# Kernel tuning notes

Hardware: AMD Instinct MI355X
Metric: run time of the kernel (lower is better)

The kernel has to match this reference:

```python
import jax, jax.numpy as jnp
import numpy as np


def _ste_round(x):
    # Round forward, identity backward (matches the custom torch Round.apply)
    return x + jax.lax.stop_gradient(jnp.round(x) - x)


def setup_inputs() -> dict:
    key = jax.random.key(0)
    k1, k2, k3 = jax.random.split(key, 3)
    N, C, H, W = 32, 256, 56, 56
    x = jax.random.normal(k1, (N, C, H, W), dtype=jnp.float32)
    # orthonormal projection basis, as produced by SVD of the covariance
    u, _ = jnp.linalg.qr(jax.random.normal(k2, (C, C), dtype=jnp.float32))
    # per-channel positive clamp values (Laplace-MSE-optimal in the original)
    clampVal = jax.random.uniform(k3, (C,), dtype=jnp.float32) * 3.0 + 0.5
    return {"x": x, "u": u, "clampVal": clampVal, "actBitwidth": 8}


def reference(x, u, clampVal, actBitwidth):
    N, C, H, W = x.shape
    # relu, then flatten to [C, N*H*W] (channels as rows, like transpose(0,1).view)
    im = jax.nn.relu(x).transpose(1, 0, 2, 3).reshape(C, -1)
    mn = jnp.mean(im, axis=1, keepdims=True)             # per-channel mean [C,1]
    im = im - mn
    # project onto PCA basis: imProj = u^T @ im  -> [C, L]
    p = jnp.matmul(u.T, im)
    # per-channel symmetric clamp (vectorized over the original per-channel loop)
    cv = clampVal[:, None]
    p = jnp.clip(p, -cv, cv)
    if actBitwidth < 17:
        dmax = jnp.max(p, axis=1, keepdims=True)         # dynamic per-channel max
        dmin = jnp.min(p, axis=1, keepdims=True)         # dynamic per-channel min
        same = dmax == dmin
        rng = jnp.where(same, jnp.ones_like(dmax), dmax - dmin)
        levels = jnp.asarray(2 ** actBitwidth - 1, dtype=p.dtype)
        scale = levels / rng
        q = _ste_round((p - dmin) * scale) / scale + dmin
        p = jnp.where(same, p, q)                        # act_quant skips if max==min
    # unproject, recenter, restore original per-channel mean
    p = jnp.matmul(u, p)
    p = p - jnp.mean(p, axis=1, keepdims=True) + mn
    return p.reshape(C, N, H, W).transpose(1, 0, 2, 3)
```

## Files before the change

### kernel.cpp

```cpp
#include <hip/hip_runtime.h>
#include <math.h>

typedef unsigned short ushort;
typedef unsigned int uint;
using half8   = __attribute__((ext_vector_type(8))) _Float16;
using short8  = __attribute__((ext_vector_type(8))) short;
using floatx4 = __attribute__((ext_vector_type(4))) float;

#define CCH   256
#define HWSZ  3136
#define NBAT  32
#define MCOLS (NBAT*HWSZ)
#define MB    784
#define NIB   4
#define GEMMGRID (MB*NIB)
#define CPX  (GEMMGRID/8)
#define QBLKS 1568

#define S_MN     0
#define S_OFFS   256
#define S_DMAX   512
#define S_DMIN   768
#define S_QSUM   1024
#define S_ROWADD 1280
#define S_MEAN   1536
#define S_TOTAL  2048

__device__ __forceinline__ ushort f2h(float f){
    _Float16 h = (_Float16)f;
    return __builtin_bit_cast(ushort, h);
}
__device__ __forceinline__ float h2f(ushort u){
    return (float)__builtin_bit_cast(_Float16, u);
}
__device__ __forceinline__ void atomicMaxF(float* addr, float v){
    if (v >= 0.f) atomicMax((int*)addr, __float_as_int(v));
    else          atomicMin((unsigned*)addr, (unsigned)__float_as_int(v));
}
__device__ __forceinline__ void atomicMinF(float* addr, float v){
    if (v >= 0.f) atomicMin((int*)addr, __float_as_int(v));
    else          atomicMax((unsigned*)addr, (unsigned)__float_as_int(v));
}
__device__ __forceinline__ void gld_lds16(const void* g, void* l){
    __builtin_amdgcn_global_load_lds((const __attribute__((address_space(1))) void*)g,
                                     (__attribute__((address_space(3))) void*)l, 16, 0, 0);
}
__device__ __forceinline__ void xcd_unswizzle(int w, int& bx, int& iy){
    int l = (w & 7)*CPX + (w >> 3);
    bx = l >> 2; iy = l & 3;
}

__global__ void k_init(float* __restrict__ stats){
    int t = blockIdx.x * 256 + threadIdx.x;
    if (t < S_TOTAL){
        float v = 0.f;
        if (t >= S_DMAX && t < S_DMIN)      v = -__builtin_inff();
        else if (t >= S_DMIN && t < S_QSUM) v =  __builtin_inff();
        stats[t] = v;
    }
}

__global__ void k_prep(const float* __restrict__ u, ushort* __restrict__ uTh){
    int i = blockIdx.x, c = threadIdx.x;
    uTh[i*CCH + c] = f2h(u[(size_t)c*CCH + i]);
}

__global__ __launch_bounds__(256) void k_trans(const float* __restrict__ x,
                                               ushort* __restrict__ xT,
                                               float* __restrict__ stats){
    __shared__ ushort tile[64*66];
    __shared__ float csum[64];
    const int hwb = blockIdx.x*64, cb = blockIdx.y*64, n = blockIdx.z;
    const int t = threadIdx.x, lane = t & 63;
    const int hw0 = (t & 15)*4;
    float4 v[4];
    #pragma unroll
    for (int pass = 0; pass < 4; ++pass){
        int c = cb + pass*16 + (t >> 4);
        v[pass] = *(const float4*)&x[((size_t)(n*CCH + c))*HWSZ + hwb + hw0];
    }
    #pragma unroll
    for (int pass = 0; pass < 4; ++pass){
        float a0 = fmaxf(v[pass].x, 0.f), a1 = fmaxf(v[pass].y, 0.f);
        float a2 = fmaxf(v[pass].z, 0.f), a3 = fmaxf(v[pass].w, 0.f);
        int cl = pass*16 + (t >> 4);
        uint p0 = (uint)f2h(a0) | ((uint)f2h(a1) << 16);
        uint p1 = (uint)f2h(a2) | ((uint)f2h(a3) << 16);
        *(uint*)&tile[cl*66 + hw0]     = p0;
        *(uint*)&tile[cl*66 + hw0 + 2] = p1;
        float sv = (a0 + a1) + (a2 + a3);
        #pragma unroll
        for (int o = 1; o < 16; o <<= 1) sv += __shfl_xor(sv, o);
        if ((lane & 15) == 0) csum[cl] = sv;
    }
    __syncthreads();
    {
        int hl = t >> 2, cs = (t & 3)*16;
        short8 o0, o1;
        #pragma unroll
        for (int j = 0; j < 8; ++j) o0[j] = (short)tile[(cs + j)*66 + hl];
        #pragma unroll
        for (int j = 0; j < 8; ++j) o1[j] = (short)tile[(cs + 8 + j)*66 + hl];
        size_t m = (size_t)n*HWSZ + hwb + hl;
        ushort* dst = xT + m*CCH + cb + cs;
        *(short8*)dst       = o0;
        *(short8*)(dst + 8) = o1;
    }
    if (t < 64) atomicAdd(&stats[S_MN + cb + t], csum[t]);
}

__global__ __launch_bounds__(256) void k_stats1(const float* __restrict__ u,
                                                float* __restrict__ stats){
    const int i = blockIdx.x, t = threadIdx.x;
    const float invM = 1.f/(float)MCOLS;
    float mnc  = stats[S_MN + t] * invM;
    float term = u[(size_t)t*CCH + i] * mnc;
    #pragma unroll
    for (int o = 1; o < 64; o <<= 1) term += __shfl_xor(term, o);
    __shared__ float red[4];
    if ((t & 63) == 0) red[t >> 6] = term;
    __syncthreads();
    if (t == 0){
        stats[S_OFFS + i] = red[0] + red[1] + red[2] + red[3];
        stats[S_MEAN + i] = stats[S_MN + i] * invM;
    }
}

__global__ __launch_bounds__(256) void k_gemm1(const ushort* __restrict__ xT,
                                               const ushort* __restrict__ uTh,
                                               const float* __restrict__ clampVal,
                                               const float* __restrict__ stats,
                                               ushort* __restrict__ pT,
                                               float* __restrict__ pmin,
                                               float* __restrict__ pmax){
    __shared__ ushort sU[64*256];
    int bx, iy; xcd_unswizzle(blockIdx.x, bx, iy);
    const int m0 = bx*128, i0 = iy*64;
    const int t = threadIdx.x, lane = t & 63, wm = t >> 6;
    const int col = lane & 15, quad = lane >> 4;
    #pragma unroll
    for (int j = 0; j < 8; ++j){
        int cid = j*256 + t;
        int row = cid >> 5, c = cid & 31;
        gld_lds16(uTh + (size_t)(i0+row)*CCH + ((c ^ (row & 7))*8), sU + cid*8);
    }
    floatx4 acc[4][2] = {};
    __syncthreads();
    const ushort* xbase = xT + (size_t)(m0 + wm*32 + col)*CCH + quad*8;
    #pragma unroll
    for (int ks = 0; ks < 8; ++ks){
        half8 b0 = __builtin_bit_cast(half8, *(const short8*)(xbase + ks*32));
        half8 b1 = __builtin_bit_cast(half8, *(const short8*)(xbase + 16*CCH + ks*32));
        #pragma unroll
        for (int fi = 0; fi < 4; ++fi){
            int chunk = (ks*4 + quad) ^ (col & 7);
            half8 a = __builtin_bit_cast(half8, *(const short8*)(sU + (fi*16 + col)*CCH + chunk*8));
            acc[fi][0] = __builtin_amdgcn_mfma_f32_16x16x32_f16(a, b0, acc[fi][0], 0, 0, 0);
            acc[fi][1] = __builtin_amdgcn_mfma_f32_16x16x32_f16(a, b1, acc[fi][1], 0, 0, 0);
        }
    }
    const int R = (iy*MB + bx)*4 + wm;
    #pragma unroll
    for (int fi = 0; fi < 4; ++fi){
        float off[4], cv[4], mnv[4], mxv[4];
        #pragma unroll
        for (int r = 0; r < 4; ++r){
            int ig = i0 + fi*16 + quad*4 + r;
            off[r] = stats[S_OFFS + ig];
            cv[r]  = clampVal[ig];
            mnv[r] =  __builtin_inff();
            mxv[r] = -__builtin_inff();
        }
        #pragma unroll
        for (int fm = 0; fm < 2; ++fm){
            int m = m0 + wm*32 + fm*16 + col;
            ushort pk[4];
            #pragma unroll
            for (int r = 0; r < 4; ++r){
                float v = acc[fi][fm][r] - off[r];
                v = fminf(fmaxf(v, -cv[r]), cv[r]);
                ushort h = f2h(v);
                float vr = h2f(h);
                pk[r] = h;
                mnv[r] = fminf(mnv[r], vr);
                mxv[r] = fmaxf(mxv[r], vr);
            }
            ushort4 q4 = make_ushort4(pk[0], pk[1], pk[2], pk[3]);
            *(ushort4*)(pT + (size_t)m*CCH + i0 + fi*16 + quad*4) = q4;
        }
        #pragma unroll
        for (int r = 0; r < 4; ++r){
            float mn = mnv[r], mx = mxv[r];
            #pragma unroll
            for (int o = 1; o < 16; o <<= 1){
                mn = fminf(mn, __shfl_xor(mn, o));
                mx = fmaxf(mx, __shfl_xor(mx, o));
            }
            if (col == 0){
                int il = fi*16 + quad*4 + r;
                pmin[(size_t)R*64 + il] = mn;
                pmax[(size_t)R*64 + il] = mx;
            }
        }
    }
}

__global__ __launch_bounds__(64) void k_mmred(const float* __restrict__ pmin,
                                              const float* __restrict__ pmax,
                                              float* __restrict__ stats){
    const int iy = blockIdx.x, sl = blockIdx.y, il = threadIdx.x;
    float mn = __builtin_inff(), mx = -__builtin_inff();
    const int base = iy*3136 + sl*98;
    for (int r = 0; r < 98; ++r){
        mn = fminf(mn, pmin[(size_t)(base + r)*64 + il]);
        mx = fmaxf(mx, pmax[(size_t)(base + r)*64 + il]);
    }
    atomicMinF(&stats[S_DMIN + iy*64 + il], mn);
    atomicMaxF(&stats[S_DMAX + iy*64 + il], mx);
}

__global__ __launch_bounds__(256) void k_prep2(const float* __restrict__ u,
                                               const int* __restrict__ abw,
                                               const float* __restrict__ stats,
                                               ushort* __restrict__ uhs){
    const int i = blockIdx.x, k = threadIdx.x;
    const int ab = *abw;
    const float lv = (float)(((ab < 17) ? (1 << ab) : 2) - 1);
    float dmax = stats[S_DMAX + k], dmin = stats[S_DMIN + k];
    float rng = dmax - dmin;
    bool cen = (ab < 17) && (ab <= 11) && (rng > 0.f);
    float step = cen ? rng / lv : 1.f;
    uhs[(size_t)i*CCH + k] = f2h(u[(size_t)i*CCH + k] * step);
}

__global__ __launch_bounds__(256) void k_qsum(ushort* __restrict__ pT,
                                              const int* __restrict__ abw,
                                              const float* __restrict__ stats,
                                              float* __restrict__ qsump){
    const int t = threadIdx.x, b = blockIdx.x;
    const int ic = (t & 31)*8, ml = t >> 5;
    const int ab = *abw;
    const float lv = (float)(((ab < 17) ? (1 << ab) : 2) - 1);
    const bool cen = (ab < 17) && (ab <= 11);
    const float hl = 0.5f * lv;
    float dmn[8], scl[8], stp[8];
    #pragma unroll
    for (int j = 0; j < 8; ++j){
        float dmax = stats[S_DMAX + ic + j], dmin = stats[S_DMIN + ic + j];
        float rng = dmax - dmin;
        bool doq = (ab < 17) && (rng > 0.f);
        scl[j] = doq ? lv / rng : 0.f;
        stp[j] = doq ? rng / lv : 0.f;
        dmn[j] = dmin;
    }
    float s[8] = {0,0,0,0,0,0,0,0};
    #pragma unroll
    for (int r = 0; r < 8; ++r){
        int m = b*64 + r*8 + ml;
        ushort* prow = pT + (size_t)m*CCH + ic;
        short8 pv = *(const short8*)prow;
        short8 ov;
        #pragma unroll
        for (int j = 0; j < 8; ++j){
            float f = h2f((ushort)pv[j]);
            float bv;
            if (scl[j] > 0.f){
                float n = rintf((f - dmn[j])*scl[j]);
                bv = cen ? (n - hl)
                         : h2f(f2h(fmaf(n, stp[j], dmn[j])));
            } else bv = f;
            ov[j] = (short)f2h(bv);
            s[j] += bv;
        }
        *(short8*)prow = ov;
    }
    __shared__ float red[256*8];
    #pragma unroll
    for (int j = 0; j < 8; ++j) red[(ic + j)*8 + ml] = s[j];
    __syncthreads();
    float tot = 0.f;
    #pragma unroll
    for (int q = 0; q < 8; ++q) tot += red[t*8 + q];
    qsump[(size_t)b*256 + t] = tot;
}

__global__ __launch_bounds__(256) void k_stats2a(const float* __restrict__ qsump,
                                                 float* __restrict__ stats){
    const int k = blockIdx.x, t = threadIdx.x;
    float s = 0.f;
    for (int b = t; b < QBLKS; b += 256) s += qsump[(size_t)b*256 + k];
    #pragma unroll
    for (int o = 1; o < 64; o <<= 1) s += __shfl_xor(s, o);
    __shared__ float red[4];
    if ((t & 63) == 0) red[t >> 6] = s;
    __syncthreads();
    if (t == 0) stats[S_QSUM + k] = (red[0]+red[1]+red[2]+red[3]) * (1.f/(float)MCOLS);
}

__global__ __launch_bounds__(256) void k_stats2b(const ushort* __restrict__ uhs,
                                                 float* __restrict__ stats){
    const int i = blockIdx.x, t = threadIdx.x;
    float term = h2f(uhs[(size_t)i*CCH + t]) * stats[S_QSUM + t];
    #pragma unroll
    for (int o = 1; o < 64; o <<= 1) term += __shfl_xor(term, o);
    __shared__ float red[4];
    if ((t & 63) == 0) red[t >> 6] = term;
    __syncthreads();
    if (t == 0) stats[S_ROWADD + i] = stats[S_MEAN + i] - (red[0]+red[1]+red[2]+red[3]);
}

__global__ __launch_bounds__(256) void k_gemm2(const ushort* __restrict__ pT,
                                               const ushort* __restrict__ uhs,
                                               float* __restrict__ out,
                                               const float* __restrict__ stats){
    __shared__ ushort sU[64*256];
    int bx, iy; xcd_unswizzle(blockIdx.x, bx, iy);
    const int m0 = bx*128, i0 = iy*64;
    const int t = threadIdx.x, lane = t & 63, wm = t >> 6;
    const int col = lane & 15, quad = lane >> 4;
    #pragma unroll
    for (int j = 0; j < 8; ++j){
        int cid = j*256 + t;
        int row = cid >> 5, c = cid & 31;
        gld_lds16(uhs + (size_t)(i0+row)*CCH + ((c ^ (row & 7))*8), sU + cid*8);
    }
    floatx4 acc[4][2] = {};
    __syncthreads();
    const ushort* pbase = pT + (size_t)(m0 + wm*32 + col)*CCH + quad*8;
    #pragma unroll
    for (int ks = 0; ks < 8; ++ks){
        half8 b0 = __builtin_bit_cast(half8, *(const short8*)(pbase + ks*32));
        half8 b1 = __builtin_bit_cast(half8, *(const short8*)(pbase + 16*CCH + ks*32));
        #pragma unroll
        for (int fi = 0; fi < 4; ++fi){
            int chunk = (ks*4 + quad) ^ (col & 7);
            half8 a = __builtin_bit_cast(half8, *(const short8*)(sU + (fi*16 + col)*CCH + chunk*8));
            acc[fi][0] = __builtin_amdgcn_mfma_f32_16x16x32_f16(a, b0, acc[fi][0], 0, 0, 0);
            acc[fi][1] = __builtin_amdgcn_mfma_f32_16x16x32_f16(a, b1, acc[fi][1], 0, 0, 0);
        }
    }
    float* sF = (float*)sU;
    const int rl = t >> 4, c4 = (t & 15)*4;
    #pragma unroll
    for (int p = 0; p < 2; ++p){
        __syncthreads();
        #pragma unroll
        for (int fi2 = 0; fi2 < 2; ++fi2){
            int il = fi2*16 + quad*4;
            #pragma unroll
            for (int fm = 0; fm < 2; ++fm){
                int ml = wm*32 + fm*16 + col;
                #pragma unroll
                for (int r = 0; r < 4; ++r)
                    sF[(il + r)*132 + ml] = acc[p*2 + fi2][fm][r];
            }
        }
        __syncthreads();
        #pragma unroll
        for (int sub = 0; sub < 2; ++sub){
            int il = sub*16 + rl;
            int ig = i0 + p*32 + il;
            float radd = stats[S_ROWADD + ig];
            #pragma unroll
            for (int v = 0; v < 2; ++v){
                int ml = c4 + v*64;
                int m = m0 + ml;
                int n = m / HWSZ, hw = m - n*HWSZ;
                float4 o;
                o.x = sF[il*132 + ml + 0] + radd;
                o.y = sF[il*132 + ml + 1] + radd;
                o.z = sF[il*132 + ml + 2] + radd;
                o.w = sF[il*132 + ml + 3] + radd;
                *(float4*)&out[((size_t)n*CCH + ig)*HWSZ + hw] = o;
            }
        }
    }
}

extern "C" void kernel_launch(void* const* d_in, const int* in_sizes, int n_in,
                              void* d_out, int out_size, void* d_ws, size_t ws_size,
                              hipStream_t stream){
    const float* x  = (const float*)d_in[0];
    const float* u  = (const float*)d_in[1];
    const float* cv = (const float*)d_in[2];
    const int*   ab = (const int*)d_in[3];
    float* out = (float*)d_out;

    ushort* pT   = (ushort*)d_ws;
    ushort* uTh  = pT + (size_t)MCOLS*CCH;
    ushort* uhs  = uTh + CCH*CCH;
    float*  stats = (float*)(uhs + CCH*CCH);

    ushort* xT   = (ushort*)d_out;
    float*  pmin = (float*)((char*)d_out + (size_t)MCOLS*CCH*2);
    float*  pmax = pmin + (size_t)NIB*MB*4*64;
    float*  qsump = pmax + (size_t)NIB*MB*4*64;

    k_init   <<<8, 256, 0, stream>>>(stats);
    k_prep   <<<256, 256, 0, stream>>>(u, uTh);
    k_trans  <<<dim3(49, 4, 32), 256, 0, stream>>>(x, xT, stats);
    k_stats1 <<<256, 256, 0, stream>>>(u, stats);
    k_gemm1  <<<GEMMGRID, 256, 0, stream>>>(xT, uTh, cv, stats, pT, pmin, pmax);
    k_mmred  <<<dim3(NIB, 32), 64, 0, stream>>>(pmin, pmax, stats);
    k_prep2  <<<256, 256, 0, stream>>>(u, ab, stats, uhs);
    k_qsum   <<<QBLKS, 256, 0, stream>>>(pT, ab, stats, qsump);
    k_stats2a<<<256, 256, 0, stream>>>(qsump, stats);
    k_stats2b<<<256, 256, 0, stream>>>(uhs, stats);
    k_gemm2  <<<GEMMGRID, 256, 0, stream>>>(pT, uhs, out, stats);
}
```

Measured before the change: 304.2 us.

## Fuse quantization into second GEMM and drop quantized write-back

The quantize step no longer writes the rounded projection back to the workspace; the second GEMM re-quantizes each fp16 operand on load using per-channel min/scale/step precomputed in the stats reduction kernel. The scaled-basis preparation is folded into the qsum kernel and stats initialization into the transpose-prep kernel, removing two launches. This removes a full read-modify-write of the large intermediate at the cost of extra ALU work and stats loads inside the GEMM inner loop.

```diff
diff --git a/kernel.cpp b/kernel.cpp
--- a/kernel.cpp
+++ b/kernel.cpp
@@ -24,7 +24,9 @@
 #define S_QSUM   1024
 #define S_ROWADD 1280
 #define S_MEAN   1536
-#define S_TOTAL  2048
+#define S_SCALE  1792
+#define S_STEP   2048
+#define S_TOTAL  2304
 
 __device__ __forceinline__ ushort f2h(float f){
     _Float16 h = (_Float16)f;
@@ -50,19 +52,19 @@
     bx = l >> 2; iy = l & 3;
 }
 
-__global__ void k_init(float* __restrict__ stats){
-    int t = blockIdx.x * 256 + threadIdx.x;
-    if (t < S_TOTAL){
-        float v = 0.f;
-        if (t >= S_DMAX && t < S_DMIN)      v = -__builtin_inff();
-        else if (t >= S_DMIN && t < S_QSUM) v =  __builtin_inff();
-        stats[t] = v;
-    }
-}
-
-__global__ void k_prep(const float* __restrict__ u, ushort* __restrict__ uTh){
+__global__ void k_prep(const float* __restrict__ u, ushort* __restrict__ uTh,
+                       float* __restrict__ stats){
     int i = blockIdx.x, c = threadIdx.x;
     uTh[i*CCH + c] = f2h(u[(size_t)c*CCH + i]);
+    if (i < 9){
+        int s = i*256 + c;
+        if (s < S_TOTAL){
+            float v = 0.f;
+            if (s >= S_DMAX && s < S_DMIN)      v = -__builtin_inff();
+            else if (s >= S_DMIN && s < S_QSUM) v =  __builtin_inff();
+            stats[s] = v;
+        }
+    }
 }
 
 __global__ __launch_bounds__(256) void k_trans(const float* __restrict__ x,
@@ -219,24 +221,12 @@
     atomicMaxF(&stats[S_DMAX + iy*64 + il], mx);
 }
 
-__global__ __launch_bounds__(256) void k_prep2(const float* __restrict__ u,
-                                               const int* __restrict__ abw,
-                                               const float* __restrict__ stats,
-                                               ushort* __restrict__ uhs){
-    const int i = blockIdx.x, k = threadIdx.x;
-    const int ab = *abw;
-    const float lv = (float)(((ab < 17) ? (1 << ab) : 2) - 1);
-    float dmax = stats[S_DMAX + k], dmin = stats[S_DMIN + k];
-    float rng = dmax - dmin;
-    bool cen = (ab < 17) && (ab <= 11) && (rng > 0.f);
-    float step = cen ? rng / lv : 1.f;
-    uhs[(size_t)i*CCH + k] = f2h(u[(size_t)i*CCH + k] * step);
-}
-
-__global__ __launch_bounds__(256) void k_qsum(ushort* __restrict__ pT,
+__global__ __launch_bounds__(256) void k_qsum(const ushort* __restrict__ pT,
+                                              const float* __restrict__ u,
                                               const int* __restrict__ abw,
                                               const float* __restrict__ stats,
-                                              float* __restrict__ qsump){
+                                              float* __restrict__ qsump,
+                                              ushort* __restrict__ uhs){
     const int t = threadIdx.x, b = blockIdx.x;
     const int ic = (t & 31)*8, ml = t >> 5;
     const int ab = *abw;
@@ -257,9 +247,7 @@
     #pragma unroll
     for (int r = 0; r < 8; ++r){
         int m = b*64 + r*8 + ml;
-        ushort* prow = pT + (size_t)m*CCH + ic;
-        short8 pv = *(const short8*)prow;
-        short8 ov;
+        short8 pv = *(const short8*)(pT + (size_t)m*CCH + ic);
         #pragma unroll
         for (int j = 0; j < 8; ++j){
             float f = h2f((ushort)pv[j]);
@@ -269,10 +257,8 @@
                 bv = cen ? (n - hl)
                          : h2f(f2h(fmaf(n, stp[j], dmn[j])));
             } else bv = f;
-            ov[j] = (short)f2h(bv);
             s[j] += bv;
         }
-        *(short8*)prow = ov;
     }
     __shared__ float red[256*8];
     #pragma unroll
@@ -282,9 +268,17 @@
     #pragma unroll
     for (int q = 0; q < 8; ++q) tot += red[t*8 + q];
     qsump[(size_t)b*256 + t] = tot;
+    if (b < 256){
+        float dmax = stats[S_DMAX + t], dmin = stats[S_DMIN + t];
+        float rng = dmax - dmin;
+        bool cenl = cen && (rng > 0.f);
+        float step = cenl ? rng / lv : 1.f;
+        uhs[(size_t)b*CCH + t] = f2h(u[(size_t)b*CCH + t] * step);
+    }
 }
 
 __global__ __launch_bounds__(256) void k_stats2a(const float* __restrict__ qsump,
+                                                 const int* __restrict__ abw,
                                                  float* __restrict__ stats){
     const int k = blockIdx.x, t = threadIdx.x;
     float s = 0.f;
@@ -294,7 +288,16 @@
     __shared__ float red[4];
     if ((t & 63) == 0) red[t >> 6] = s;
     __syncthreads();
-    if (t == 0) stats[S_QSUM + k] = (red[0]+red[1]+red[2]+red[3]) * (1.f/(float)MCOLS);
+    if (t == 0){
+        stats[S_QSUM + k] = (red[0]+red[1]+red[2]+red[3]) * (1.f/(float)MCOLS);
+        int ab = *abw;
+        float lv = (float)(((ab < 17) ? (1 << ab) : 2) - 1);
+        float dmax = stats[S_DMAX + k], dmin = stats[S_DMIN + k];
+        float rng = dmax - dmin;
+        bool doq = (ab < 17) && (rng > 0.f);
+        stats[S_SCALE + k] = doq ? lv / rng : 0.f;
+        stats[S_STEP + k]  = doq ? rng / lv : 0.f;
+    }
 }
 
 __global__ __launch_bounds__(256) void k_stats2b(const ushort* __restrict__ uhs,
@@ -311,6 +314,7 @@
 
 __global__ __launch_bounds__(256) void k_gemm2(const ushort* __restrict__ pT,
                                                const ushort* __restrict__ uhs,
+                                               const int* __restrict__ abw,
                                                float* __restrict__ out,
                                                const float* __restrict__ stats){
     __shared__ ushort sU[64*256];
@@ -324,19 +328,59 @@
         int row = cid >> 5, c = cid & 31;
         gld_lds16(uhs + (size_t)(i0+row)*CCH + ((c ^ (row & 7))*8), sU + cid*8);
     }
+    const int ab = *abw;
+    const float lv = (float)(((ab < 17) ? (1 << ab) : 2) - 1);
+    const bool cen = (ab < 17) && (ab <= 11);
+    const float hl = 0.5f * lv;
     floatx4 acc[4][2] = {};
     __syncthreads();
     const ushort* pbase = pT + (size_t)(m0 + wm*32 + col)*CCH + quad*8;
     #pragma unroll
     for (int ks = 0; ks < 8; ++ks){
-        half8 b0 = __builtin_bit_cast(half8, *(const short8*)(pbase + ks*32));
-        half8 b1 = __builtin_bit_cast(half8, *(const short8*)(pbase + 16*CCH + ks*32));
+        const int w0 = ks*32 + quad*8;
+        float dmn[8], scl[8];
+        *(float4*)&dmn[0] = *(const float4*)&stats[S_DMIN  + w0];
+        *(float4*)&dmn[4] = *(const float4*)&stats[S_DMIN  + w0 + 4];
+        *(float4*)&scl[0] = *(const float4*)&stats[S_SCALE + w0];
+        *(float4*)&scl[4] = *(const float4*)&stats[S_SCALE + w0 + 4];
+        half8 b[2];
+        if (cen){
+            #pragma unroll
+            for (int fm = 0; fm < 2; ++fm){
+                short8 pv = *(const short8*)(pbase + fm*16*CCH + ks*32);
+                #pragma unroll
+                for (int j = 0; j < 8; ++j){
+                    float f = h2f((ushort)pv[j]);
+                    float n = rintf((f - dmn[j])*scl[j]);
+                    float bv = (scl[j] > 0.f) ? (n - hl) : f;
+                    b[fm][j] = (_Float16)bv;
+                }
+            }
+        } else {
+            float stp[8];
+            *(float4*)&stp[0] = *(const float4*)&stats[S_STEP + w0];
+            *(float4*)&stp[4] = *(const float4*)&stats[S_STEP + w0 + 4];
+            #pragma unroll
+            for (int fm = 0; fm < 2; ++fm){
+                short8 pv = *(const short8*)(pbase + fm*16*CCH + ks*32);
+                #pragma unroll
+                for (int j = 0; j < 8; ++j){
+                    float f = h2f((ushort)pv[j]);
+                    float bv = f;
+                    if (scl[j] > 0.f){
+                        float n = rintf((f - dmn[j])*scl[j]);
+                        bv = h2f(f2h(fmaf(n, stp[j], dmn[j])));
+                    }
+                    b[fm][j] = (_Float16)bv;
+                }
+            }
+        }
         #pragma unroll
         for (int fi = 0; fi < 4; ++fi){
             int chunk = (ks*4 + quad) ^ (col & 7);
             half8 a = __builtin_bit_cast(half8, *(const short8*)(sU + (fi*16 + col)*CCH + chunk*8));
-            acc[fi][0] = __builtin_amdgcn_mfma_f32_16x16x32_f16(a, b0, acc[fi][0], 0, 0, 0);
-            acc[fi][1] = __builtin_amdgcn_mfma_f32_16x16x32_f16(a, b1, acc[fi][1], 0, 0, 0);
+            acc[fi][0] = __builtin_amdgcn_mfma_f32_16x16x32_f16(a, b[0], acc[fi][0], 0, 0, 0);
+            acc[fi][1] = __builtin_amdgcn_mfma_f32_16x16x32_f16(a, b[1], acc[fi][1], 0, 0, 0);
         }
     }
     float* sF = (float*)sU;
@@ -396,15 +440,13 @@
     float*  pmax = pmin + (size_t)NIB*MB*4*64;
     float*  qsump = pmax + (size_t)NIB*MB*4*64;
 
-    k_init   <<<8, 256, 0, stream>>>(stats);
-    k_prep   <<<256, 256, 0, stream>>>(u, uTh);
+    k_prep   <<<256, 256, 0, stream>>>(u, uTh, stats);
     k_trans  <<<dim3(49, 4, 32), 256, 0, stream>>>(x, xT, stats);
     k_stats1 <<<256, 256, 0, stream>>>(u, stats);
     k_gemm1  <<<GEMMGRID, 256, 0, stream>>>(xT, uTh, cv, stats, pT, pmin, pmax);
     k_mmred  <<<dim3(NIB, 32), 64, 0, stream>>>(pmin, pmax, stats);
-    k_prep2  <<<256, 256, 0, stream>>>(u, ab, stats, uhs);
-    k_qsum   <<<QBLKS, 256, 0, stream>>>(pT, ab, stats, qsump);
-    k_stats2a<<<256, 256, 0, stream>>>(qsump, stats);
+    k_qsum   <<<QBLKS, 256, 0, stream>>>(pT, u, ab, stats, qsump, uhs);
+    k_stats2a<<<256, 256, 0, stream>>>(qsump, ab, stats);
     k_stats2b<<<256, 256, 0, stream>>>(uhs, stats);
-    k_gemm2  <<<GEMMGRID, 256, 0, stream>>>(pT, uhs, out, stats);
-}
+    k_gemm2  <<<GEMMGRID, 256, 0, stream>>>(pT, uhs, ab, out, stats);
+}
```

Result: slower. 314.3 us (+3.3%).
